# Kernel tuning notes

Hardware: AMD Instinct MI355X
Metric: run time of the kernel (lower is better)

## Reference

```python
import jax, jax.numpy as jnp
import numpy as np

EPS = 1e-12


def setup_inputs() -> dict:
    key = jax.random.key(0)
    k = jax.random.split(key, 6)
    B, C, T, A = 8, 1536, 4096, 128
    x = jax.random.normal(k[0], (B, C, T), dtype=jnp.float32)
    lengths = jax.random.randint(k[1], (B,), T // 2, T + 1, dtype=jnp.int64)
    W1 = jax.random.normal(k[2], (A, 3 * C), dtype=jnp.float32) * (1.0 / np.sqrt(3 * C))
    b1 = jax.random.normal(k[3], (A,), dtype=jnp.float32) * 0.01
    W2 = jax.random.normal(k[4], (1, A), dtype=jnp.float32) * (1.0 / np.sqrt(A))
    b2 = jax.random.normal(k[5], (1,), dtype=jnp.float32) * 0.01
    return {"x": x, "lengths": lengths, "W1": W1, "b1": b1, "W2": W2, "b2": b2}


def reference(x, lengths, W1, b1, W2, b2):
    # x: [B, C, T]
    B, C, T = x.shape
    mask = (jnp.arange(T)[None, :] < lengths[:, None]).astype(x.dtype)  # [B, T]
    m3 = mask[:, None, :]  # [B, 1, T]

    # causal (cumulative) mean / std for global context
    count = jnp.clip(jnp.cumsum(mask, axis=1), 1.0)[:, None, :]        # [B, 1, T]
    causal_mean = jnp.cumsum(x * m3, axis=2) / count                   # [B, C, T]
    causal_var = jnp.cumsum(x * x * m3, axis=2) / count - causal_mean ** 2
    causal_std = jnp.sqrt(jnp.clip(causal_var, EPS))

    attn_in = jnp.concatenate([x, causal_mean, causal_std], axis=1)    # [B, 3C, T]
    attn_in = attn_in.transpose(0, 2, 1)                               # [B, T, 3C]

    h = jnp.tanh(attn_in @ W1.T + b1)                                  # [B, T, A]
    logits = (h @ W2.T + b2)[..., 0]                                   # [B, T]

    # logits are query-independent, so causal softmax row q is
    # exp(l_k) / cumsum(exp(l))_q for k <= q -> O(T*C) prefix scan.
    e = jnp.exp(logits - jnp.max(logits, axis=1, keepdims=True))       # [B, T]
    Z = jnp.cumsum(e, axis=1)[:, None, :]                              # [B, 1, T]
    ew = e[:, None, :]                                                 # [B, 1, T]

    weighted_mean = jnp.cumsum(ew * x, axis=2) / Z                     # [B, C, T]
    sq_diff = (x - weighted_mean) ** 2
    weighted_var = jnp.cumsum(ew * sq_diff, axis=2) / Z
    weighted_std = jnp.sqrt(jnp.clip(weighted_var, EPS))

    # each causal softmax row sums to 1 -> final weights are 1/(T+eps)
    fw = 1.0 / (jnp.asarray(T, x.dtype) + EPS)
    final_mean = jnp.sum(weighted_mean, axis=2) * fw                   # [B, C]
    final_std = jnp.sum(weighted_std, axis=2) * fw
    return jnp.concatenate([final_mean, final_std], axis=1)            # [B, 2C]
```

## Files before the change

kernel.cpp:

```cpp
#include <hip/hip_runtime.h>
#include <hip/hip_bf16.h>

#define B_ 8
#define C_ 1536
#define T_ 4096
#define A_ 128
#define K3_ 4608
#define M32_ 128
#define KP_ 200

typedef _Float16 h8  __attribute__((ext_vector_type(8)));
typedef _Float16 h2v __attribute__((ext_vector_type(2)));
typedef float    f4  __attribute__((ext_vector_type(4)));

__global__ void k0_pack(const float* __restrict__ W1, _Float16* __restrict__ W1f) {
    int i = blockIdx.x * 256 + threadIdx.x;
    if (i >= A_ * K3_) return;
    int a = i / K3_, k = i - a * K3_;
    int t8 = a >> 4, r15 = a & 15;
    int kb = k >> 5, q = (k >> 3) & 3, j = k & 7;
    int lane = q * 16 + r15;
    W1f[(size_t)((kb * 8 + t8) * 64 + lane) * 8 + j] = (_Float16)W1[i];
}

__global__ __launch_bounds__(256) void k1_carry(
    const float* __restrict__ x, const int* __restrict__ lens,
    float2* __restrict__ carry)
{
    const int rowid = blockIdx.x * 4 + (threadIdx.x >> 6);
    const int lane  = threadIdx.x & 63;
    const int b     = rowid / C_;
    const int len   = lens[b];
    const float* xr = x + (size_t)rowid * T_ + lane * 64;
    const int tbase = lane * 64;
    float s1 = 0.f, s2 = 0.f, h1 = 0.f, h2 = 0.f;
#pragma unroll
    for (int g = 0; g < 16; ++g) {
        float4 v = *(const float4*)(xr + g * 4);
        float vs[4] = {v.x, v.y, v.z, v.w};
#pragma unroll
        for (int j = 0; j < 4; ++j) {
            float xv = vs[j];
            float vm = (tbase + g * 4 + j < len) ? xv : 0.f;
            s1 += vm; s2 += vm * xv;
        }
        if (g == 7) { h1 = s1; h2 = s2; }
    }
    float V1 = s1, V2 = s2;
#pragma unroll
    for (int d = 1; d < 64; d <<= 1) {
        float o1 = __shfl_up(V1, d, 64);
        float o2 = __shfl_up(V2, d, 64);
        if (lane >= d) { V1 += o1; V2 += o2; }
    }
    const float b1e = V1 - s1, b2e = V2 - s2;
    float2* cp = carry + (size_t)rowid * M32_ + lane * 2;
    cp[0] = make_float2(b1e, b2e);
    cp[1] = make_float2(b1e + h1, b2e + h2);
}

__global__ __launch_bounds__(256) void k2_gemm(
    const float* __restrict__ x, const int* __restrict__ lens,
    const float2* __restrict__ carry, const _Float16* __restrict__ W1f,
    const float* __restrict__ b1, const float* __restrict__ W2,
    float* __restrict__ logits)
{
    __shared__ _Float16 tile[32][KP_];
    __shared__ float s_w2[A_], s_b1[A_];
    __shared__ float lpart[2][32];

    const int tid = threadIdx.x;
    const int i    = blockIdx.x;
    const int mlow = i >> 7;
    const int b    = (i >> 4) & 7;
    const int m    = ((i & 15) << 3) | mlow;
    const int t0   = m << 5;
    const int len  = lens[b];

    if (tid < A_) { s_w2[tid] = W2[tid]; s_b1[tid] = b1[tid]; }

    const int cp  = tid >> 3;
    const int sgm = tid & 7;
    const int tb  = t0 + sgm * 4;

    const int lane = tid & 63;
    const int w    = tid >> 6;
    const int mtg  = w & 1;
    const int ntg  = w >> 1;
    const int ln15 = lane & 15, q = lane >> 4;
    const h8* W1f8 = (const h8*)W1f;

    f4 acc[4] = {};

    for (int c0 = 0; c0 < C_; c0 += 64) {
        const size_t rowA = (size_t)b * C_ + c0 + cp * 2;
        const float* xpA = x + rowA * T_ + tb;
        float4 va = *(const float4*)xpA;
        float4 vb = *(const float4*)(xpA + T_);
        float xa[4] = {va.x, va.y, va.z, va.w};
        float xb[4] = {vb.x, vb.y, vb.z, vb.w};
        float pA1[4], pA2[4], pB1[4], pB2[4];
        float a1 = 0.f, a2 = 0.f, c1 = 0.f, c2 = 0.f;
#pragma unroll
        for (int j = 0; j < 4; ++j) {
            bool in = (tb + j) < len;
            float ma = in ? xa[j] : 0.f;
            float mb = in ? xb[j] : 0.f;
            a1 += ma; a2 += ma * xa[j]; pA1[j] = a1; pA2[j] = a2;
            c1 += mb; c2 += mb * xb[j]; pB1[j] = c1; pB2[j] = c2;
        }
        float t1 = a1, t2 = a2, t3 = c1, t4 = c2;
#pragma unroll
        for (int d = 1; d < 8; d <<= 1) {
            float o1 = __shfl_up(t1, d, 8);
            float o2 = __shfl_up(t2, d, 8);
            float o3 = __shfl_up(t3, d, 8);
            float o4 = __shfl_up(t4, d, 8);
            if (sgm >= d) { t1 += o1; t2 += o2; t3 += o3; t4 += o4; }
        }
        const float eA1 = t1 - a1, eA2 = t2 - a2;
        const float eB1 = t3 - c1, eB2 = t4 - c2;
        const float2 crA = carry[rowA * M32_ + m];
        const float2 crB = carry[(rowA + 1) * M32_ + m];
        const int cb = cp >> 2;
        const int co = (cp & 3) * 2;
#pragma unroll
        for (int j = 0; j < 4; ++j) {
            const int t  = tb + j;
            const int tl = sgm * 4 + j;
            float fn = (float)min(t + 1, len);
            float rn = __builtin_amdgcn_rcpf(fn);
            float S1a = crA.x + eA1 + pA1[j];
            float S2a = crA.y + eA2 + pA2[j];
            float mA = S1a * rn;
            float vA = S2a * rn - mA * mA;
            float dA = sqrtf(fmaxf(vA, 1e-12f));
            float S1b = crB.x + eB1 + pB1[j];
            float S2b = crB.y + eB2 + pB2[j];
            float mB = S1b * rn;
            float vB = S2b * rn - mB * mB;
            float dB = sqrtf(fmaxf(vB, 1e-12f));
            const int s  = (tl >> 3) & 3;
            const int xo = ((cb ^ s) << 3) + co;
            h2v px = {(_Float16)xa[j], (_Float16)xb[j]};
            h2v pm = {(_Float16)mA, (_Float16)mB};
            h2v pd = {(_Float16)dA, (_Float16)dB};
            *(h2v*)&tile[tl][xo]       = px;
            *(h2v*)&tile[tl][64 + xo]  = pm;
            *(h2v*)&tile[tl][128 + xo] = pd;
        }
        __syncthreads();
        const int tl = ntg * 16 + ln15;
        const int s  = (tl >> 3) & 3;
        const int kb0 = c0 >> 5;
#pragma unroll
        for (int p = 0; p < 3; ++p) {
#pragma unroll
            for (int kk = 0; kk < 2; ++kk) {
                const int bb = (kk * 4 + q) ^ s;
                h8 bf = *(const h8*)&tile[tl][p * 64 + bb * 8];
                const int kbp = p * 48 + kb0 + kk;
#pragma unroll
                for (int ii = 0; ii < 4; ++ii) {
                    h8 af = W1f8[(kbp * 8 + mtg * 4 + ii) * 64 + lane];
                    acc[ii] = __builtin_amdgcn_mfma_f32_16x16x32_f16(af, bf, acc[ii], 0, 0, 0);
                }
            }
        }
        __syncthreads();
    }
    float pr = 0.f;
#pragma unroll
    for (int ii = 0; ii < 4; ++ii) {
#pragma unroll
        for (int rg = 0; rg < 4; ++rg) {
            int a = (mtg * 4 + ii) * 16 + q * 4 + rg;
            float h = acc[ii][rg] + s_b1[a];
            pr += tanhf(h) * s_w2[a];
        }
    }
    pr += __shfl_xor(pr, 16, 64);
    pr += __shfl_xor(pr, 32, 64);
    if (q == 0) lpart[mtg][ntg * 16 + ln15] = pr;
    __syncthreads();
    if (tid < 32) {
        logits[(size_t)b * T_ + t0 + tid] = lpart[0][tid] + lpart[1][tid];
    }
}

__global__ __launch_bounds__(64) void k3_softmax(
    const float* __restrict__ logits, float* __restrict__ earr,
    float* __restrict__ zarr)
{
    const int b = blockIdx.x;
    const int l = threadIdx.x;
    const float* base = logits + (size_t)b * T_ + l * 64;
    float lg[64];
#pragma unroll
    for (int ii = 0; ii < 16; ++ii) {
        float4 v = *(const float4*)(base + ii * 4);
        lg[ii * 4 + 0] = v.x; lg[ii * 4 + 1] = v.y;
        lg[ii * 4 + 2] = v.z; lg[ii * 4 + 3] = v.w;
    }
    float mx = -3.4e38f;
#pragma unroll
    for (int i = 0; i < 64; ++i) mx = fmaxf(mx, lg[i]);
#pragma unroll
    for (int d = 1; d < 64; d <<= 1) mx = fmaxf(mx, __shfl_xor(mx, d, 64));
    float tot = 0.f;
#pragma unroll
    for (int i = 0; i < 64; ++i) { lg[i] = expf(lg[i] - mx); tot += lg[i]; }
    float V = tot;
#pragma unroll
    for (int d = 1; d < 64; d <<= 1) {
        float o = __shfl_up(V, d, 64);
        if (l >= d) V += o;
    }
    float run = V - tot;
    float* eo = earr + (size_t)b * T_ + l * 64;
    float* zo = zarr + (size_t)b * T_ + l * 64;
#pragma unroll
    for (int ii = 0; ii < 16; ++ii) {
        float4 ev, zv;
        float e0 = lg[ii * 4 + 0]; run += e0; ev.x = e0; zv.x = run;
        float e1 = lg[ii * 4 + 1]; run += e1; ev.y = e1; zv.y = run;
        float e2 = lg[ii * 4 + 2]; run += e2; ev.z = e2; zv.z = run;
        float e3 = lg[ii * 4 + 3]; run += e3; ev.w = e3; zv.w = run;
        *(float4*)(eo + ii * 4) = ev;
        *(float4*)(zo + ii * 4) = zv;
    }
}

__global__ __launch_bounds__(256) void k4_wstats(
    const float* __restrict__ x, const float* __restrict__ earr,
    const float* __restrict__ zarr, float* __restrict__ out)
{
    const int rowid = blockIdx.x * 4 + (threadIdx.x >> 6);
    const int lane  = threadIdx.x & 63;
    const int b = rowid / C_;
    const int c = rowid - b * C_;
    const float* xr = x + (size_t)rowid * T_ + lane * 64;
    const float* er = earr + (size_t)b * T_ + lane * 64;
    const float* zr = zarr + (size_t)b * T_ + lane * 64;

    float xs[64];
    float stot = 0.f;
#pragma unroll
    for (int g = 0; g < 16; ++g) {
        float4 xv = *(const float4*)(xr + g * 4);
        float4 ev = *(const float4*)(er + g * 4);
        xs[g * 4 + 0] = xv.x; xs[g * 4 + 1] = xv.y;
        xs[g * 4 + 2] = xv.z; xs[g * 4 + 3] = xv.w;
        stot += ev.x * xv.x + ev.y * xv.y + ev.z * xv.z + ev.w * xv.w;
    }
    float V = stot;
#pragma unroll
    for (int d = 1; d < 64; d <<= 1) {
        float o = __shfl_up(V, d, 64);
        if (lane >= d) V += o;
    }
    const float Sbase = V - stot;
    float am = 0.f, pw = 0.f, pd = 0.f;
#pragma unroll
    for (int g = 0; g < 16; ++g) {
        float4 ev = *(const float4*)(er + g * 4);
        float4 zv = *(const float4*)(zr + g * 4);
        float pe[4] = {ev.x, ev.y, ev.z, ev.w};
        float pz[4] = {zv.x, zv.y, zv.z, zv.w};
#pragma unroll
        for (int j = 0; j < 4; ++j) {
            float xv = xs[g * 4 + j];
            pw += pe[j] * xv;
            float wm = (Sbase + pw) * __builtin_amdgcn_rcpf(pz[j]);
            am += wm;
            float df = xv - wm;
            pd += pe[j] * df * df;
        }
    }
    float V2 = pd;
#pragma unroll
    for (int d = 1; d < 64; d <<= 1) {
        float o = __shfl_up(V2, d, 64);
        if (lane >= d) V2 += o;
    }
    const float Dbase = V2 - pd;
    float asd = 0.f; pw = 0.f; pd = 0.f;
#pragma unroll
    for (int g = 0; g < 16; ++g) {
        float4 ev = *(const float4*)(er + g * 4);
        float4 zv = *(const float4*)(zr + g * 4);
        float pe[4] = {ev.x, ev.y, ev.z, ev.w};
        float pz[4] = {zv.x, zv.y, zv.z, zv.w};
#pragma unroll
        for (int j = 0; j < 4; ++j) {
            float xv = xs[g * 4 + j];
            float rz = __builtin_amdgcn_rcpf(pz[j]);
            pw += pe[j] * xv;
            float wm = (Sbase + pw) * rz;
            float df = xv - wm;
            pd += pe[j] * df * df;
            float var = (Dbase + pd) * rz;
            asd += sqrtf(fmaxf(var, 1e-12f));
        }
    }
#pragma unroll
    for (int d = 1; d < 64; d <<= 1) {
        am  += __shfl_xor(am, d, 64);
        asd += __shfl_xor(asd, d, 64);
    }
    if (lane == 0) {
        out[(size_t)b * (2 * C_) + c]      = am  * (1.f / 4096.f);
        out[(size_t)b * (2 * C_) + C_ + c] = asd * (1.f / 4096.f);
    }
}

extern "C" void kernel_launch(void* const* d_in, const int* in_sizes, int n_in,
                              void* d_out, int out_size, void* d_ws, size_t ws_size,
                              hipStream_t stream) {
    const float* x    = (const float*)d_in[0];
    const int*   lens = (const int*)d_in[1];
    const float* W1   = (const float*)d_in[2];
    const float* b1   = (const float*)d_in[3];
    const float* W2   = (const float*)d_in[4];
    float* out = (float*)d_out;

    char* ws = (char*)d_ws;
    float2*    carry  = (float2*)ws;
    _Float16*  W1f    = (_Float16*)(ws + 12582912);
    float*     logits = (float*)(ws + 13762560);
    float*     earr   = (float*)(ws + 13893632);
    float*     zarr   = (float*)(ws + 14024704);

    k0_pack   <<<(A_ * K3_ + 255) / 256, 256, 0, stream>>>(W1, W1f);
    k1_carry  <<<(B_ * C_) / 4, 256, 0, stream>>>(x, lens, carry);
    k2_gemm   <<<B_ * M32_, 256, 0, stream>>>(x, lens, carry, W1f, b1, W2, logits);
    k3_softmax<<<B_, 64, 0, stream>>>(logits, earr, zarr);
    k4_wstats <<<(B_ * C_) / 4, 256, 0, stream>>>(x, earr, zarr, out);
}
```

Before: 478.1 us.

## Switch carry and weighted-stats kernels to coalesced chunked scans with running bases

Both the carry kernel and the weighted-stats kernel previously gave each lane a contiguous 64-element slice, so every load instruction was strided by 256 bytes across lanes. They now walk the row in 256-element chunks with lane-contiguous float4 loads, doing a wave scan per chunk and carrying a running base. This removes the 64-float register array in k4 and the repeated passes over e and z. The carry kernel also skips loads for chunks past the sequence length. The cost is many more shuffle scans per row, 16 chunks times one or two 6-step scans.

```diff
diff --git a/kernel.cpp b/kernel.cpp
--- a/kernel.cpp
+++ b/kernel.cpp
@@ -31,32 +31,52 @@
     const int lane  = threadIdx.x & 63;
     const int b     = rowid / C_;
     const int len   = lens[b];
-    const float* xr = x + (size_t)rowid * T_ + lane * 64;
-    const int tbase = lane * 64;
-    float s1 = 0.f, s2 = 0.f, h1 = 0.f, h2 = 0.f;
+    const float* xr = x + (size_t)rowid * T_;
+    float2* cp = carry + (size_t)rowid * M32_;
+
+    const int grp = lane >> 3;
+    float base1 = 0.f, base2 = 0.f;
+
 #pragma unroll
     for (int g = 0; g < 16; ++g) {
-        float4 v = *(const float4*)(xr + g * 4);
-        float vs[4] = {v.x, v.y, v.z, v.w};
-#pragma unroll
-        for (int j = 0; j < 4; ++j) {
-            float xv = vs[j];
-            float vm = (tbase + g * 4 + j < len) ? xv : 0.f;
-            s1 += vm; s2 += vm * xv;
-        }
-        if (g == 7) { h1 = s1; h2 = s2; }
-    }
-    float V1 = s1, V2 = s2;
-#pragma unroll
-    for (int d = 1; d < 64; d <<= 1) {
-        float o1 = __shfl_up(V1, d, 64);
-        float o2 = __shfl_up(V2, d, 64);
-        if (lane >= d) { V1 += o1; V2 += o2; }
-    }
-    const float b1e = V1 - s1, b2e = V2 - s2;
-    float2* cp = carry + (size_t)rowid * M32_ + lane * 2;
-    cp[0] = make_float2(b1e, b2e);
-    cp[1] = make_float2(b1e + h1, b2e + h2);
+        const int t0g = g * 256;
+        if (t0g >= len) {
+            if ((lane & 7) == 0) cp[g * 8 + grp] = make_float2(base1, base2);
+            continue;
+        }
+        float4 v = *(const float4*)(xr + t0g + lane * 4);
+        float s1, s2;
+        if (t0g + 256 <= len) {
+            s1 = v.x + v.y + v.z + v.w;
+            s2 = v.x * v.x + v.y * v.y + v.z * v.z + v.w * v.w;
+        } else {
+            const int tb = t0g + lane * 4;
+            float vs[4] = {v.x, v.y, v.z, v.w};
+            s1 = 0.f; s2 = 0.f;
+#pragma unroll
+            for (int j = 0; j < 4; ++j) {
+                float m = (tb + j < len) ? vs[j] : 0.f;
+                s1 += m; s2 += m * vs[j];
+            }
+        }
+        float g1 = s1, g2 = s2;
+        g1 += __shfl_xor(g1, 1, 64); g2 += __shfl_xor(g2, 1, 64);
+        g1 += __shfl_xor(g1, 2, 64); g2 += __shfl_xor(g2, 2, 64);
+        g1 += __shfl_xor(g1, 4, 64); g2 += __shfl_xor(g2, 4, 64);
+        float V1 = g1, V2 = g2;
+#pragma unroll
+        for (int d = 8; d < 64; d <<= 1) {
+            float o1 = __shfl_up(V1, d, 64);
+            float o2 = __shfl_up(V2, d, 64);
+            if (lane >= d) { V1 += o1; V2 += o2; }
+        }
+        const float e1 = V1 - g1, e2 = V2 - g2;
+        if ((lane & 7) == 0) {
+            cp[g * 8 + grp] = make_float2(base1 + e1, base2 + e2);
+        }
+        base1 += __shfl(V1, 63, 64);
+        base2 += __shfl(V2, 63, 64);
+    }
 }
 
 __global__ __launch_bounds__(256) void k2_gemm(
@@ -239,69 +259,62 @@
     const int lane  = threadIdx.x & 63;
     const int b = rowid / C_;
     const int c = rowid - b * C_;
-    const float* xr = x + (size_t)rowid * T_ + lane * 64;
-    const float* er = earr + (size_t)b * T_ + lane * 64;
-    const float* zr = zarr + (size_t)b * T_ + lane * 64;
-
-    float xs[64];
-    float stot = 0.f;
+    const float* xr = x + (size_t)rowid * T_;
+    const float* er = earr + (size_t)b * T_;
+    const float* zr = zarr + (size_t)b * T_;
+
+    float am = 0.f, asd = 0.f;
+    float baseS = 0.f, baseD = 0.f;
+
 #pragma unroll
     for (int g = 0; g < 16; ++g) {
-        float4 xv = *(const float4*)(xr + g * 4);
-        float4 ev = *(const float4*)(er + g * 4);
-        xs[g * 4 + 0] = xv.x; xs[g * 4 + 1] = xv.y;
-        xs[g * 4 + 2] = xv.z; xs[g * 4 + 3] = xv.w;
-        stot += ev.x * xv.x + ev.y * xv.y + ev.z * xv.z + ev.w * xv.w;
-    }
-    float V = stot;
-#pragma unroll
-    for (int d = 1; d < 64; d <<= 1) {
-        float o = __shfl_up(V, d, 64);
-        if (lane >= d) V += o;
-    }
-    const float Sbase = V - stot;
-    float am = 0.f, pw = 0.f, pd = 0.f;
-#pragma unroll
-    for (int g = 0; g < 16; ++g) {
-        float4 ev = *(const float4*)(er + g * 4);
-        float4 zv = *(const float4*)(zr + g * 4);
-        float pe[4] = {ev.x, ev.y, ev.z, ev.w};
-        float pz[4] = {zv.x, zv.y, zv.z, zv.w};
-#pragma unroll
-        for (int j = 0; j < 4; ++j) {
-            float xv = xs[g * 4 + j];
-            pw += pe[j] * xv;
-            float wm = (Sbase + pw) * __builtin_amdgcn_rcpf(pz[j]);
-            am += wm;
-            float df = xv - wm;
-            pd += pe[j] * df * df;
-        }
-    }
-    float V2 = pd;
-#pragma unroll
-    for (int d = 1; d < 64; d <<= 1) {
-        float o = __shfl_up(V2, d, 64);
-        if (lane >= d) V2 += o;
-    }
-    const float Dbase = V2 - pd;
-    float asd = 0.f; pw = 0.f; pd = 0.f;
-#pragma unroll
-    for (int g = 0; g < 16; ++g) {
-        float4 ev = *(const float4*)(er + g * 4);
-        float4 zv = *(const float4*)(zr + g * 4);
-        float pe[4] = {ev.x, ev.y, ev.z, ev.w};
-        float pz[4] = {zv.x, zv.y, zv.z, zv.w};
-#pragma unroll
-        for (int j = 0; j < 4; ++j) {
-            float xv = xs[g * 4 + j];
-            float rz = __builtin_amdgcn_rcpf(pz[j]);
-            pw += pe[j] * xv;
-            float wm = (Sbase + pw) * rz;
-            float df = xv - wm;
-            pd += pe[j] * df * df;
-            float var = (Dbase + pd) * rz;
-            asd += sqrtf(fmaxf(var, 1e-12f));
-        }
+        const int off = g * 256 + lane * 4;
+        float4 xv = *(const float4*)(xr + off);
+        float4 ev = *(const float4*)(er + off);
+        float4 zv = *(const float4*)(zr + off);
+        float s0 = ev.x * xv.x;
+        float s1 = s0 + ev.y * xv.y;
+        float s2 = s1 + ev.z * xv.z;
+        float s3 = s2 + ev.w * xv.w;
+        float V = s3;
+#pragma unroll
+        for (int d = 1; d < 64; d <<= 1) {
+            float o = __shfl_up(V, d, 64);
+            if (lane >= d) V += o;
+        }
+        const float Sx = baseS + (V - s3);
+        baseS += __shfl(V, 63, 64);
+        const float rz0 = __builtin_amdgcn_rcpf(zv.x);
+        const float rz1 = __builtin_amdgcn_rcpf(zv.y);
+        const float rz2 = __builtin_amdgcn_rcpf(zv.z);
+        const float rz3 = __builtin_amdgcn_rcpf(zv.w);
+        const float wm0 = (Sx + s0) * rz0;
+        const float wm1 = (Sx + s1) * rz1;
+        const float wm2 = (Sx + s2) * rz2;
+        const float wm3 = (Sx + s3) * rz3;
+        am += (wm0 + wm1) + (wm2 + wm3);
+        const float d0 = xv.x - wm0;
+        const float d1 = xv.y - wm1;
+        const float d2 = xv.z - wm2;
+        const float d3 = xv.w - wm3;
+        float q0 = ev.x * d0 * d0;
+        float q1 = q0 + ev.y * d1 * d1;
+        float q2 = q1 + ev.z * d2 * d2;
+        float q3 = q2 + ev.w * d3 * d3;
+        float W = q3;
+#pragma unroll
+        for (int d = 1; d < 64; d <<= 1) {
+            float o = __shfl_up(W, d, 64);
+            if (lane >= d) W += o;
+        }
+        const float Dx = baseD + (W - q3);
+        baseD += __shfl(W, 63, 64);
+        const float v0 = (Dx + q0) * rz0;
+        const float v1 = (Dx + q1) * rz1;
+        const float v2 = (Dx + q2) * rz2;
+        const float v3 = (Dx + q3) * rz3;
+        asd += (sqrtf(fmaxf(v0, 1e-12f)) + sqrtf(fmaxf(v1, 1e-12f)))
+             + (sqrtf(fmaxf(v2, 1e-12f)) + sqrtf(fmaxf(v3, 1e-12f)));
     }
 #pragma unroll
     for (int d = 1; d < 64; d <<= 1) {
```

Measured after the change: 446.3 us. 1.07x faster.
